# Optimization experiments

Hardware: AMD Instinct MI355X
Metric: run time of the kernel (lower is better)

The kernel has to match this reference:

```python
import jax, jax.numpy as jnp
import numpy as np
from jax import lax

EPS = 1e-5

def _conv1d(x, w, b):
    # x: [B,C,L], w: [O,I,K], valid padding, stride 1
    y = lax.conv_general_dilated(x, w, window_strides=(1,), padding='VALID',
                                 dimension_numbers=('NCH', 'OIH', 'NCH'))
    return y + b[None, :, None]

def setup_inputs() -> dict:
    key = jax.random.key(0)
    ks = jax.random.split(key, 7)
    B, L, C = 16, 4096, 512
    x = jax.random.normal(ks[0], (B, L, C), dtype=jnp.float32)
    fan3 = 1.0 / np.sqrt(C * 3)
    fan1 = 1.0 / np.sqrt(C * 1)
    w_down = jax.random.uniform(ks[1], (C, C, 3), jnp.float32, -fan3, fan3)
    b_down = jax.random.uniform(ks[2], (C,), jnp.float32, -fan3, fan3)
    w_pad = jax.random.uniform(ks[3], (C, C, 1), jnp.float32, -fan1, fan1)
    b_pad = jax.random.uniform(ks[4], (C,), jnp.float32, -fan1, fan1)
    gamma = jnp.ones((C,), jnp.float32)
    beta = jnp.zeros((C,), jnp.float32)
    return {"x": x, "w_down": w_down, "b_down": b_down,
            "w_pad": w_pad, "b_pad": b_pad, "gamma": gamma, "beta": beta}

def reference(x, w_down, b_down, w_pad, b_pad, gamma, beta):
    # d == 2 branch of ConvLayer
    B, L, C = x.shape

    def branch(xs):  # xs: [B, L//2, C]
        xt = jnp.transpose(xs, (0, 2, 1))                 # [B,C,L/2]
        p1 = _conv1d(xt, w_down, b_down)                  # [B,C,L/2-2]
        p2 = _conv1d(xt[:, :, :2], w_pad, b_pad)          # [B,C,2]
        return jnp.concatenate([p1, p2], axis=2)          # [B,C,L/2]

    x1_p = branch(x[:, 0::2, :])
    x2_p = branch(x[:, 1::2, :])
    # interleave: even positions from x1_p, odd from x2_p
    x_p = jnp.stack([x1_p, x2_p], axis=3).reshape(B, C, L)

    # BatchNorm1d in training mode: batch stats over (batch, length)
    mean = jnp.mean(x_p, axis=(0, 2), keepdims=True)
    var = jnp.var(x_p, axis=(0, 2), keepdims=True)
    xn = (x_p - mean) * lax.rsqrt(var + EPS)
    xn = xn * gamma[None, :, None] + beta[None, :, None]

    y = jax.nn.elu(xn)                                    # dropout = identity (eval)
    y = y + jnp.transpose(x, (0, 2, 1))                   # residual [B,C,L]

    # MaxPool1d(kernel=3, stride=2, padding=1)
    yp = jnp.pad(y, ((0, 0), (0, 0), (1, 1)), constant_values=-jnp.inf)
    pooled = lax.reduce_window(yp, -jnp.inf, lax.max, (1, 1, 3), (1, 1, 2), 'VALID')
    return jnp.transpose(pooled, (0, 2, 1))               # [B, L//2, C]
```

## Files before the change

### kernel.cpp

```cpp
#include <hip/hip_runtime.h>
#include <hip/hip_bf16.h>
#include <math.h>

typedef __bf16 bf16;
typedef __bf16 bf16x8 __attribute__((ext_vector_type(8)));
typedef float floatx4 __attribute__((ext_vector_type(4)));

#define GAS __attribute__((address_space(1)))
#define LAS __attribute__((address_space(3)))

static constexpr int B_ = 16, L_ = 4096, C_ = 512;
static constexpr int M_ = B_ * L_;
static constexpr int K_ = 3 * C_;

__global__ void prep(const float* __restrict__ x, bf16* __restrict__ xb,
                     const float* __restrict__ wd, bf16* __restrict__ wr) {
    if (blockIdx.x < 16384) {
        const size_t i = ((size_t)blockIdx.x * 256 + threadIdx.x) * 8;
        floatx4 a = *(const floatx4*)(x + i);
        floatx4 b = *(const floatx4*)(x + i + 4);
        bf16x8 o;
#pragma unroll
        for (int j = 0; j < 4; ++j) { o[j] = (bf16)a[j]; o[4 + j] = (bf16)b[j]; }
        *(bf16x8*)(xb + i) = o;
    } else {
        int idx = (blockIdx.x - 16384) * 256 + threadIdx.x;
        int o   = idx / K_;
        int rem = idx - o * K_;
        int kk  = rem >> 9;
        int i   = rem & 511;
        wr[idx] = (bf16)wd[o * K_ + i * 3 + kk];
    }
}

__global__ __launch_bounds__(512, 2) void gemm_conv(
    const bf16* __restrict__ x, const bf16* __restrict__ wr,
    const float* __restrict__ bd, bf16* __restrict__ xp, float* __restrict__ sums)
{
    __shared__ bf16 As[256 * 64];
    __shared__ bf16 Bs[256 * 64];

    const int tid = threadIdx.x;
    const int u   = blockIdx.x;
    const int mb  = (u & 7) + 8 * (u >> 4);
    const int nb  = (u >> 3) & 1;
    const int m0  = mb * 256;
    const int n0  = nb * 256;

    const int wave = tid >> 6;
    const int lane = tid & 63;
    const int wm = wave & 3;
    const int wn = wave >> 2;
    const int tm = lane & 15;
    const int quad = lane >> 4;

    floatx4 acc[4][8];
#pragma unroll
    for (int i = 0; i < 4; ++i)
#pragma unroll
        for (int j = 0; j < 8; ++j) acc[i][j] = floatx4{0.f, 0.f, 0.f, 0.f};

    int srow[4], ssc[4];
#pragma unroll
    for (int j = 0; j < 4; ++j) {
        const int qa = tid + 512 * j;
        srow[j] = qa >> 3;
        ssc[j]  = (qa & 7) ^ (srow[j] & 7);
    }

    for (int kt = 0; kt < 24; ++kt) {
        const int kk = kt >> 3;
        const int i0 = (kt & 7) << 6;
#pragma unroll
        for (int j = 0; j < 4; ++j) {
            int sr = m0 + srow[j] + 2 * kk; if (sr > M_ - 1) sr = M_ - 1;
            const bf16* sa = x + (size_t)sr * C_ + i0 + ssc[j] * 8;
            __builtin_amdgcn_global_load_lds((const GAS void*)sa,
                (LAS void*)(As + (tid + 512 * j) * 8), 16, 0, 0);
            const bf16* sb = wr + (size_t)(n0 + srow[j]) * K_ + kk * C_ + i0 + ssc[j] * 8;
            __builtin_amdgcn_global_load_lds((const GAS void*)sb,
                (LAS void*)(Bs + (tid + 512 * j) * 8), 16, 0, 0);
        }
        __syncthreads();

#pragma unroll
        for (int ksel = 0; ksel < 2; ++ksel) {
            const int xo = ((ksel * 4 + quad) ^ (tm & 7)) << 3;
            bf16x8 af[4], bfr[8];
#pragma unroll
            for (int mi = 0; mi < 4; ++mi) {
                const int r = wm * 64 + mi * 16 + tm;
                af[mi] = *(const bf16x8*)(As + r * 64 + xo);
            }
#pragma unroll
            for (int ni = 0; ni < 8; ++ni) {
                const int r = wn * 128 + ni * 16 + tm;
                bfr[ni] = *(const bf16x8*)(Bs + r * 64 + xo);
            }
#pragma unroll
            for (int mi = 0; mi < 4; ++mi)
#pragma unroll
                for (int ni = 0; ni < 8; ++ni)
                    acc[mi][ni] = __builtin_amdgcn_mfma_f32_16x16x32_bf16(af[mi], bfr[ni], acc[mi][ni], 0, 0, 0);
        }
        __syncthreads();
    }

    float bias[8];
#pragma unroll
    for (int ni = 0; ni < 8; ++ni) bias[ni] = bd[n0 + wn * 128 + ni * 16 + tm];

    float s[8] = {0,0,0,0,0,0,0,0}, q[8] = {0,0,0,0,0,0,0,0};
#pragma unroll
    for (int mi = 0; mi < 4; ++mi) {
#pragma unroll
        for (int r = 0; r < 4; ++r) {
            const int m = m0 + wm * 64 + mi * 16 + quad * 4 + r;
            const bool valid = (m & (L_ - 1)) < L_ - 4;
            bf16* dst = xp + (size_t)m * C_ + n0 + wn * 128 + tm;
#pragma unroll
            for (int ni = 0; ni < 8; ++ni) {
                const float v = acc[mi][ni][r] + bias[ni];
                dst[ni * 16] = (bf16)v;
                if (valid) { s[ni] += v; q[ni] += v * v; }
            }
        }
    }
#pragma unroll
    for (int ni = 0; ni < 8; ++ni) {
        float sv = s[ni], qv = q[ni];
        sv += __shfl_xor(sv, 16); sv += __shfl_xor(sv, 32);
        qv += __shfl_xor(qv, 16); qv += __shfl_xor(qv, 32);
        if (quad == 0) {
            const int c = n0 + wn * 128 + ni * 16 + tm;
            atomicAdd(&sums[c], sv);
            atomicAdd(&sums[C_ + c], qv);
        }
    }
}

__global__ void fixup(const float* __restrict__ x, const float* __restrict__ wp,
                      const float* __restrict__ bp, bf16* __restrict__ xp,
                      float* __restrict__ sums)
{
    const int b = blockIdx.x >> 2;
    const int j = blockIdx.x & 3;
    __shared__ float xrow[C_];
    for (int i = threadIdx.x; i < C_; i += 256)
        xrow[i] = x[(size_t)(b * L_ + j) * C_ + i];
    __syncthreads();
    for (int c = threadIdx.x; c < C_; c += 256) {
        const float* w = wp + (size_t)c * C_;
        float acc = 0.f;
#pragma unroll 4
        for (int i = 0; i < C_; i += 4) {
            floatx4 wv = *(const floatx4*)(w + i);
#pragma unroll
            for (int u = 0; u < 4; ++u) acc += wv[u] * xrow[i + u];
        }
        const float v = acc + bp[c];
        xp[(size_t)(b * L_ + 4092 + j) * C_ + c] = (bf16)v;
        atomicAdd(&sums[c], v);
        atomicAdd(&sums[C_ + c], v * v);
    }
}

__global__ void final_pool(const bf16* __restrict__ xp, const bf16* __restrict__ xb,
                           const float* __restrict__ sums, const float* __restrict__ gamma,
                           const float* __restrict__ beta, float* __restrict__ out)
{
    const int gid = blockIdx.x * 256 + threadIdx.x;
    const int cg = gid & 63;
    const int t  = (gid >> 6) & 2047;
    const int b  = gid >> 17;
    const int c0 = cg << 3;

    float sc[8], sh[8];
    const float invn = 1.0f / 65536.0f;
#pragma unroll
    for (int j = 0; j < 8; ++j) {
        const int c = c0 + j;
        float mean = sums[c] * invn;
        float var  = sums[C_ + c] * invn - mean * mean;
        float scale = gamma[c] * rsqrtf(var + 1e-5f);
        sc[j] = scale;
        sh[j] = beta[c] - mean * scale;
    }

    float best[8];
#pragma unroll
    for (int j = 0; j < 8; ++j) best[j] = -INFINITY;

#pragma unroll
    for (int dl = -1; dl <= 1; ++dl) {
        const int l = 2 * t + dl;
        if (l < 0) continue;
        const size_t off = (size_t)(b * L_ + l) * C_ + c0;
        bf16x8 xpv = *(const bf16x8*)(xp + off);
        bf16x8 xv  = *(const bf16x8*)(xb + off);
#pragma unroll
        for (int j = 0; j < 8; ++j) {
            float z = sc[j] * (float)xpv[j] + sh[j];
            float y = (z > 0.f) ? z : (__expf(z) - 1.f);
            y += (float)xv[j];
            best[j] = fmaxf(best[j], y);
        }
    }
    floatx4 o0, o1;
#pragma unroll
    for (int j = 0; j < 4; ++j) { o0[j] = best[j]; o1[j] = best[4 + j]; }
    *(floatx4*)(out + (size_t)gid * 8) = o0;
    *(floatx4*)(out + (size_t)gid * 8 + 4) = o1;
}

extern "C" void kernel_launch(void* const* d_in, const int* in_sizes, int n_in,
                              void* d_out, int out_size, void* d_ws, size_t ws_size,
                              hipStream_t stream)
{
    const float* x      = (const float*)d_in[0];
    const float* w_down = (const float*)d_in[1];
    const float* b_down = (const float*)d_in[2];
    const float* w_pad  = (const float*)d_in[3];
    const float* b_pad  = (const float*)d_in[4];
    const float* gamma  = (const float*)d_in[5];
    const float* beta   = (const float*)d_in[6];
    float* out = (float*)d_out;

    char* ws = (char*)d_ws;
    bf16*  xb   = (bf16*)ws;
    bf16*  xp   = (bf16*)(ws + (size_t)M_ * C_ * 2);
    bf16*  wr   = (bf16*)(ws + (size_t)M_ * C_ * 4);
    float* sums = (float*)(ws + (size_t)M_ * C_ * 4 + (size_t)C_ * K_ * 2);

    hipMemsetAsync(sums, 0, 2 * C_ * sizeof(float), stream);
    prep<<<dim3(16384 + 3072), dim3(256), 0, stream>>>(x, xb, w_down, wr);
    gemm_conv<<<dim3(512), dim3(512), 0, stream>>>(xb, wr, b_down, xp, sums);
    fixup<<<dim3(64), dim3(256), 0, stream>>>(x, w_pad, b_pad, xp, sums);
    final_pool<<<dim3(8192), dim3(256), 0, stream>>>(xp, xb, sums, gamma, beta, out);
}
```

Measured before the change: 416.4 us.

## Double-buffer GEMM LDS tiles and remap wave layout to 2x4

Adds a two-stage LDS double buffer so the global-to-LDS loads for the next K tile overlap the MFMA work on the current one, using manual vmcnt waits and raw barriers. The wave grid changes from 4x2 to 2x4 (each wave now computes 128x64), fragment offsets are precomputed, and MFMA sections get raised scheduling priority. LDS use doubles to 128 KB per block, which may limit occupancy to one block per CU despite launch_bounds(512,2). The hand-written waitcnt and barrier sequence is fragile if the compiler reorders loads.

Measured after the change: 394.1 us. 1.06x faster.

```diff
diff --git a/kernel.cpp b/kernel.cpp
--- a/kernel.cpp
+++ b/kernel.cpp
@@ -37,8 +37,8 @@
     const bf16* __restrict__ x, const bf16* __restrict__ wr,
     const float* __restrict__ bd, bf16* __restrict__ xp, float* __restrict__ sums)
 {
-    __shared__ bf16 As[256 * 64];
-    __shared__ bf16 Bs[256 * 64];
+    __shared__ bf16 As[2 * 256 * 64];
+    __shared__ bf16 Bs[2 * 256 * 64];
 
     const int tid = threadIdx.x;
     const int u   = blockIdx.x;
@@ -49,16 +49,16 @@
 
     const int wave = tid >> 6;
     const int lane = tid & 63;
-    const int wm = wave & 3;
-    const int wn = wave >> 2;
+    const int wm = wave & 1;
+    const int wn = wave >> 1;
     const int tm = lane & 15;
     const int quad = lane >> 4;
 
-    floatx4 acc[4][8];
-#pragma unroll
-    for (int i = 0; i < 4; ++i)
-#pragma unroll
-        for (int j = 0; j < 8; ++j) acc[i][j] = floatx4{0.f, 0.f, 0.f, 0.f};
+    floatx4 acc[8][4];
+#pragma unroll
+    for (int i = 0; i < 8; ++i)
+#pragma unroll
+        for (int j = 0; j < 4; ++j) acc[i][j] = floatx4{0.f, 0.f, 0.f, 0.f};
 
     int srow[4], ssc[4];
 #pragma unroll
@@ -68,58 +68,97 @@
         ssc[j]  = (qa & 7) ^ (srow[j] & 7);
     }
 
-    for (int kt = 0; kt < 24; ++kt) {
-        const int kk = kt >> 3;
-        const int i0 = (kt & 7) << 6;
+    const int xo0 = (quad ^ (tm & 7)) << 3;
+    const int xo1 = ((4 + quad) ^ (tm & 7)) << 3;
+    int aoff[8], boff[4];
+#pragma unroll
+    for (int mi = 0; mi < 8; ++mi) aoff[mi] = (wm * 128 + mi * 16 + tm) * 64;
+#pragma unroll
+    for (int ni = 0; ni < 4; ++ni) boff[ni] = (wn * 64 + ni * 16 + tm) * 64;
+
+    auto stage = [&](int t, int b) {
+        const int kk = t >> 3;
+        const int i0 = (t & 7) << 6;
+        bf16* Ad = As + b * (256 * 64);
+        bf16* Bd = Bs + b * (256 * 64);
 #pragma unroll
         for (int j = 0; j < 4; ++j) {
             int sr = m0 + srow[j] + 2 * kk; if (sr > M_ - 1) sr = M_ - 1;
             const bf16* sa = x + (size_t)sr * C_ + i0 + ssc[j] * 8;
             __builtin_amdgcn_global_load_lds((const GAS void*)sa,
-                (LAS void*)(As + (tid + 512 * j) * 8), 16, 0, 0);
+                (LAS void*)(Ad + (tid + 512 * j) * 8), 16, 0, 0);
             const bf16* sb = wr + (size_t)(n0 + srow[j]) * K_ + kk * C_ + i0 + ssc[j] * 8;
             __builtin_amdgcn_global_load_lds((const GAS void*)sb,
-                (LAS void*)(Bs + (tid + 512 * j) * 8), 16, 0, 0);
-        }
-        __syncthreads();
-
-#pragma unroll
-        for (int ksel = 0; ksel < 2; ++ksel) {
-            const int xo = ((ksel * 4 + quad) ^ (tm & 7)) << 3;
-            bf16x8 af[4], bfr[8];
-#pragma unroll
-            for (int mi = 0; mi < 4; ++mi) {
-                const int r = wm * 64 + mi * 16 + tm;
-                af[mi] = *(const bf16x8*)(As + r * 64 + xo);
-            }
-#pragma unroll
-            for (int ni = 0; ni < 8; ++ni) {
-                const int r = wn * 128 + ni * 16 + tm;
-                bfr[ni] = *(const bf16x8*)(Bs + r * 64 + xo);
-            }
-#pragma unroll
-            for (int mi = 0; mi < 4; ++mi)
-#pragma unroll
-                for (int ni = 0; ni < 8; ++ni)
-                    acc[mi][ni] = __builtin_amdgcn_mfma_f32_16x16x32_bf16(af[mi], bfr[ni], acc[mi][ni], 0, 0, 0);
-        }
-        __syncthreads();
-    }
-
-    float bias[8];
-#pragma unroll
-    for (int ni = 0; ni < 8; ++ni) bias[ni] = bd[n0 + wn * 128 + ni * 16 + tm];
-
-    float s[8] = {0,0,0,0,0,0,0,0}, q[8] = {0,0,0,0,0,0,0,0};
-#pragma unroll
-    for (int mi = 0; mi < 4; ++mi) {
+                (LAS void*)(Bd + (tid + 512 * j) * 8), 16, 0, 0);
+        }
+    };
+
+    auto compute = [&](const bf16* Ab, const bf16* Bb) {
+        bf16x8 bfr[2][4];
+#pragma unroll
+        for (int kh = 0; kh < 2; ++kh)
+#pragma unroll
+            for (int ni = 0; ni < 4; ++ni)
+                bfr[kh][ni] = *(const bf16x8*)(Bb + boff[ni] + (kh ? xo1 : xo0));
+#pragma unroll
+        for (int mq = 0; mq < 2; ++mq) {
+            bf16x8 afr[2][4];
+#pragma unroll
+            for (int kh = 0; kh < 2; ++kh)
+#pragma unroll
+                for (int mi = 0; mi < 4; ++mi)
+                    afr[kh][mi] = *(const bf16x8*)(Ab + aoff[mq * 4 + mi] + (kh ? xo1 : xo0));
+            __builtin_amdgcn_s_setprio(1);
+#pragma unroll
+            for (int kh = 0; kh < 2; ++kh)
+#pragma unroll
+                for (int mi = 0; mi < 4; ++mi)
+#pragma unroll
+                    for (int ni = 0; ni < 4; ++ni)
+                        acc[mq * 4 + mi][ni] = __builtin_amdgcn_mfma_f32_16x16x32_bf16(
+                            afr[kh][mi], bfr[kh][ni], acc[mq * 4 + mi][ni], 0, 0, 0);
+            __builtin_amdgcn_s_setprio(0);
+        }
+    };
+
+    stage(0, 0);
+    stage(1, 1);
+    asm volatile("s_waitcnt vmcnt(8)" ::: "memory");
+    asm volatile("s_barrier" ::: "memory");
+
+    for (int kt2 = 0; kt2 < 22; kt2 += 2) {
+        compute(As, Bs);
+        asm volatile("s_barrier" ::: "memory");
+        stage(kt2 + 2, 0);
+        asm volatile("s_waitcnt vmcnt(8)" ::: "memory");
+        asm volatile("s_barrier" ::: "memory");
+
+        compute(As + 256 * 64, Bs + 256 * 64);
+        asm volatile("s_barrier" ::: "memory");
+        stage(kt2 + 3, 1);
+        asm volatile("s_waitcnt vmcnt(8)" ::: "memory");
+        asm volatile("s_barrier" ::: "memory");
+    }
+    compute(As, Bs);
+    asm volatile("s_barrier" ::: "memory");
+    asm volatile("s_waitcnt vmcnt(0)" ::: "memory");
+    asm volatile("s_barrier" ::: "memory");
+    compute(As + 256 * 64, Bs + 256 * 64);
+
+    float bias[4];
+#pragma unroll
+    for (int ni = 0; ni < 4; ++ni) bias[ni] = bd[n0 + wn * 64 + ni * 16 + tm];
+
+    float s[4] = {0, 0, 0, 0}, q[4] = {0, 0, 0, 0};
+#pragma unroll
+    for (int mi = 0; mi < 8; ++mi) {
 #pragma unroll
         for (int r = 0; r < 4; ++r) {
-            const int m = m0 + wm * 64 + mi * 16 + quad * 4 + r;
+            const int m = m0 + wm * 128 + mi * 16 + quad * 4 + r;
             const bool valid = (m & (L_ - 1)) < L_ - 4;
-            bf16* dst = xp + (size_t)m * C_ + n0 + wn * 128 + tm;
-#pragma unroll
-            for (int ni = 0; ni < 8; ++ni) {
+            bf16* dst = xp + (size_t)m * C_ + n0 + wn * 64 + tm;
+#pragma unroll
+            for (int ni = 0; ni < 4; ++ni) {
                 const float v = acc[mi][ni][r] + bias[ni];
                 dst[ni * 16] = (bf16)v;
                 if (valid) { s[ni] += v; q[ni] += v * v; }
@@ -127,12 +166,12 @@
         }
     }
 #pragma unroll
-    for (int ni = 0; ni < 8; ++ni) {
+    for (int ni = 0; ni < 4; ++ni) {
         float sv = s[ni], qv = q[ni];
         sv += __shfl_xor(sv, 16); sv += __shfl_xor(sv, 32);
         qv += __shfl_xor(qv, 16); qv += __shfl_xor(qv, 32);
         if (quad == 0) {
-            const int c = n0 + wn * 128 + ni * 16 + tm;
+            const int c = n0 + wn * 64 + ni * 16 + tm;
             atomicAdd(&sums[c], sv);
             atomicAdd(&sums[C_ + c], qv);
         }
```
